# Kernel optimization log

Measured on AMD Instinct MI355X. Metric: run time of the kernel, lower is better.

## Reference

```python
import jax, jax.numpy as jnp
import numpy as np

B, L, H, D = 2, 2048, 16, 64
HID = H * D
EPS = 1e-6


def setup_inputs() -> dict:
    key = jax.random.key(0)
    k1, k2, k3 = jax.random.split(key, 3)
    x = jax.random.normal(k1, (B, L, HID), dtype=jnp.float32)
    Wqkv = jax.random.normal(k2, (HID, 3 * HID), dtype=jnp.float32) * 0.02
    Wo = jax.random.normal(k3, (HID, HID), dtype=jnp.float32) * 0.02
    q_norm_w = jnp.ones((D,), dtype=jnp.float32)
    k_norm_w = jnp.ones((D,), dtype=jnp.float32)
    # real RoPE tables: (L, D/2)
    d2 = D // 2
    inv_freq = 1.0 / (10000.0 ** (np.arange(d2, dtype=np.float32) / d2))
    ang = np.arange(L, dtype=np.float32)[:, None] * inv_freq[None, :]
    cos = jnp.asarray(np.cos(ang), dtype=jnp.float32)
    sin = jnp.asarray(np.sin(ang), dtype=jnp.float32)
    return {"x": x, "Wqkv": Wqkv, "Wo": Wo, "q_norm_w": q_norm_w,
            "k_norm_w": k_norm_w, "cos": cos, "sin": sin}


def _rmsnorm(t, w, eps=EPS):
    # normalize over last (head_dim) axis
    var = jnp.mean(t * t, axis=-1, keepdims=True)
    return t * jax.lax.rsqrt(var + eps) * w


def _rope(t, cos, sin):
    # t: (B,H,L,D); cos,sin: (1,1,L,D/2)
    d2 = t.shape[-1] // 2
    t1, t2 = t[..., :d2], t[..., d2:]
    return jnp.concatenate([t1 * cos - t2 * sin, t1 * sin + t2 * cos], axis=-1)


def reference(x, Wqkv, Wo, q_norm_w, k_norm_w, cos, sin):
    Bx, Lx, _ = x.shape
    qkv = x @ Wqkv                                   # (B,L,3*HID)
    qkv = qkv.reshape(Bx, Lx, 3, H, D)
    q = jnp.transpose(qkv[:, :, 0], (0, 2, 1, 3))    # (B,H,L,D)
    k = jnp.transpose(qkv[:, :, 1], (0, 2, 1, 3))
    v = jnp.transpose(qkv[:, :, 2], (0, 2, 1, 3))
    q = _rmsnorm(q, q_norm_w)
    k = _rmsnorm(k, k_norm_w)
    c = cos[:Lx][None, None]                         # (1,1,L,D/2)
    s = sin[:Lx][None, None]
    q = _rope(q, c, s)
    k = _rope(k, c, s)
    scale = 1.0 / jnp.sqrt(jnp.float32(D))
    scores = jnp.einsum("bhqd,bhkd->bhqk", q, k) * scale
    causal = jnp.tril(jnp.ones((Lx, Lx), dtype=bool))
    scores = jnp.where(causal, scores, jnp.finfo(scores.dtype).min)
    attn = jax.nn.softmax(scores, axis=-1)
    out = jnp.einsum("bhqk,bhkd->bhqd", attn, v)     # (B,H,L,D)
    out = jnp.transpose(out, (0, 2, 1, 3)).reshape(Bx, Lx, HID)
    return out @ Wo
```

## Files before the change

### kernel.cpp

```cpp
#include <hip/hip_runtime.h>
#include <hip/hip_bf16.h>

typedef __attribute__((ext_vector_type(8))) short bh8;
typedef __attribute__((ext_vector_type(4))) float f4;

typedef unsigned short u16;
typedef unsigned int u32;

__device__ inline u16 f2b(float f) {
  __hip_bfloat16 h = __float2bfloat16(f);
  union { __hip_bfloat16 h; u16 u; } v; v.h = h; return v.u;
}
__device__ inline float b2f(u16 b) {
  union { u32 u; float f; } v; v.u = ((u32)b) << 16;
  return v.f;
}

__device__ __forceinline__ void gload16(const u16* g, u16* l) {
  __builtin_amdgcn_global_load_lds(
      (__attribute__((address_space(1))) void*)(g),
      (__attribute__((address_space(3))) void*)(l),
      16, 0, 0);
}

__global__ __launch_bounds__(256) void k_prep1(const float* __restrict__ x,
                                               const float* __restrict__ Wqkv,
                                               const float* __restrict__ Wo,
                                               u16* __restrict__ xb,
                                               u16* __restrict__ wqkvT,
                                               u16* __restrict__ woT) {
  int idx = blockIdx.x;
  if (idx < 4096) {
    int i = (idx * 256 + threadIdx.x) * 4;
    float4 v = *(const float4*)&x[i];
    ushort4 o;
    o.x = f2b(v.x); o.y = f2b(v.y); o.z = f2b(v.z); o.w = f2b(v.w);
    *(ushort4*)&xb[i] = o;
    return;
  }
  __shared__ u16 t[32][33];
  const float* W; u16* WT; int K, N, bxi, byi;
  if (idx < 7168) {
    int id2 = idx - 4096;
    W = Wqkv; WT = wqkvT; K = 1024; N = 3072;
    bxi = id2 % 96; byi = id2 / 96;
  } else {
    int id2 = idx - 7168;
    W = Wo; WT = woT; K = 1024; N = 1024;
    bxi = id2 & 31; byi = id2 >> 5;
  }
  int bx = bxi * 32, by = byi * 32;
  int xx = threadIdx.x & 31, yy = threadIdx.x >> 5;
  for (int j = 0; j < 4; ++j) {
    int r = yy + j * 8;
    t[r][xx] = f2b(W[(size_t)(by + r) * N + bx + xx]);
  }
  __syncthreads();
  for (int j = 0; j < 4; ++j) {
    int r = yy + j * 8;
    WT[(size_t)(bx + r) * K + by + xx] = t[xx][r];
  }
}

template <bool F32OUT>
__global__ __launch_bounds__(256) void k_gemm(const u16* __restrict__ A,
                                              const u16* __restrict__ Bt,
                                              void* __restrict__ Cout,
                                              int M, int N, int K) {
  __shared__ u16 As[2][128 * 64];
  __shared__ u16 Bs[2][128 * 64];
  const int tid = threadIdx.x;
  const int lane = tid & 63, wid = tid >> 6;
  const int l15 = lane & 15, lg = lane >> 4;

  int nwg = gridDim.x * gridDim.y;
  int bid = blockIdx.y * gridDim.x + blockIdx.x;
  int cpx = nwg >> 3;
  int swz = (bid & 7) * cpx + (bid >> 3);
  int bx = swz % gridDim.x, by = swz / gridDim.x;
  const int bm = bx * 128, bn = by * 128;
  const int wr = (wid >> 1) * 64, wc = (wid & 1) * 64;

  f4 acc[4][4] = {};

  const int srow = wid * 32 + (lane >> 3);
  const int scol = (lane & 7) * 8;
  const u16* gA = A  + (size_t)(bm + srow) * K + scol;
  const u16* gB = Bt + (size_t)(bn + srow) * K + scol;

  const int nk = K >> 6;

  {
    const u16* ga = gA; const u16* gb = gB;
    u16* la = &As[0][(wid * 32) * 64];
    u16* lb = &Bs[0][(wid * 32) * 64];
    #pragma unroll
    for (int c = 0; c < 4; ++c) {
      gload16(ga, la);
      gload16(gb, lb);
      ga += (size_t)8 * K; gb += (size_t)8 * K;
      la += 8 * 64;        lb += 8 * 64;
    }
  }
  __syncthreads();

  for (int t = 0; t < nk; ++t) {
    if (t + 1 < nk) {
      int kb = (t + 1) << 6;
      const u16* ga = gA + kb; const u16* gb = gB + kb;
      u16* la = &As[(t + 1) & 1][(wid * 32) * 64];
      u16* lb = &Bs[(t + 1) & 1][(wid * 32) * 64];
      #pragma unroll
      for (int c = 0; c < 4; ++c) {
        gload16(ga, la);
        gload16(gb, lb);
        ga += (size_t)8 * K; gb += (size_t)8 * K;
        la += 8 * 64;        lb += 8 * 64;
      }
    }
    const u16* as = &As[t & 1][0];
    const u16* bs = &Bs[t & 1][0];
    #pragma unroll
    for (int kk = 0; kk < 2; ++kk) {
      bh8 a[4], b[4];
      #pragma unroll
      for (int m = 0; m < 4; ++m)
        a[m] = *(const bh8*)&as[(wr + m * 16 + l15) * 64 + kk * 32 + lg * 8];
      #pragma unroll
      for (int n = 0; n < 4; ++n)
        b[n] = *(const bh8*)&bs[(wc + n * 16 + l15) * 64 + kk * 32 + lg * 8];
      #pragma unroll
      for (int m = 0; m < 4; ++m)
        #pragma unroll
        for (int n = 0; n < 4; ++n)
          acc[m][n] = __builtin_amdgcn_mfma_f32_16x16x32_bf16(a[m], b[n], acc[m][n], 0, 0, 0);
    }
    __syncthreads();
  }

  for (int m = 0; m < 4; ++m)
    for (int n = 0; n < 4; ++n)
      for (int r = 0; r < 4; ++r) {
        int row = bm + wr + m * 16 + lg * 4 + r;
        int col = bn + wc + n * 16 + l15;
        float v = acc[m][n][r];
        if constexpr (F32OUT) ((float*)Cout)[(size_t)row * N + col] = v;
        else                  ((u16*)Cout)[(size_t)row * N + col]  = f2b(v);
      }
}

__global__ __launch_bounds__(256) void k_prep2(const u16* __restrict__ qkv,
                                               const float* __restrict__ qw,
                                               const float* __restrict__ kw,
                                               const float* __restrict__ cosp,
                                               const float* __restrict__ sinp,
                                               u16* __restrict__ Q,
                                               u16* __restrict__ K,
                                               u16* __restrict__ Vt) {
  const float CSC = 0.125f * 1.44269504088896f;
  int idx = blockIdx.x;
  if (idx < 2048) {
    int wid = threadIdx.x >> 6, lane = threadIdx.x & 63;
    int gw = idx * 4 + wid;
    int isK = gw & 1;
    int bl = gw >> 1;
    int l = bl & 2047, b = bl >> 11;
    int h = lane >> 2, qd = lane & 3;
    const u16* src = qkv + (size_t)bl * 3072 + isK * 1024 + h * 64 + qd * 8;
    bh8 t1 = *(const bh8*)src;
    bh8 t2 = *(const bh8*)(src + 32);
    float a1[8], a2[8];
    float ss = 0.0f;
    #pragma unroll
    for (int j = 0; j < 8; ++j) {
      a1[j] = b2f((u16)t1[j]); a2[j] = b2f((u16)t2[j]);
      ss += a1[j] * a1[j] + a2[j] * a2[j];
    }
    ss += __shfl_xor(ss, 1, 64);
    ss += __shfl_xor(ss, 2, 64);
    float rr = rsqrtf(ss * (1.0f / 64.0f) + 1e-6f);
    const float* wt = isK ? kw : qw;
    float w1[8], w2[8], cc[8], sn[8];
    *(float4*)&w1[0] = *(const float4*)&wt[qd * 8];
    *(float4*)&w1[4] = *(const float4*)&wt[qd * 8 + 4];
    *(float4*)&w2[0] = *(const float4*)&wt[32 + qd * 8];
    *(float4*)&w2[4] = *(const float4*)&wt[32 + qd * 8 + 4];
    *(float4*)&cc[0] = *(const float4*)&cosp[l * 32 + qd * 8];
    *(float4*)&cc[4] = *(const float4*)&cosp[l * 32 + qd * 8 + 4];
    *(float4*)&sn[0] = *(const float4*)&sinp[l * 32 + qd * 8];
    *(float4*)&sn[4] = *(const float4*)&sinp[l * 32 + qd * 8 + 4];
    float scl = isK ? 1.0f : CSC;
    bh8 o1, o2;
    #pragma unroll
    for (int j = 0; j < 8; ++j) {
      float x1 = a1[j] * rr * w1[j];
      float x2 = a2[j] * rr * w2[j];
      o1[j] = (short)f2b((x1 * cc[j] - x2 * sn[j]) * scl);
      o2[j] = (short)f2b((x1 * sn[j] + x2 * cc[j]) * scl);
    }
    u16* dst = (isK ? K : Q) + ((size_t)(b * 16 + h) * 2048 + l) * 64 + qd * 8;
    *(bh8*)dst = o1;
    *(bh8*)(dst + 32) = o2;
  } else {
    __shared__ u16 t[32][33];
    int v = idx - 2048;
    int bxi = v & 63, byi = (v >> 6) & 1, bh = v >> 7;
    int b = bh >> 4, h = bh & 15;
    int lb = bxi * 32, db = byi * 32;
    int xx = threadIdx.x & 31, yy = threadIdx.x >> 5;
    const u16* src = qkv + (size_t)b * 2048 * 3072 + 2048 + h * 64;
    for (int j = 0; j < 4; ++j) {
      int r = yy + j * 8;
      t[r][xx] = src[(size_t)(lb + r) * 3072 + db + xx];
    }
    __syncthreads();
    u16* dst = Vt + (size_t)bh * 64 * 2048;
    for (int j = 0; j < 4; ++j) {
      int r = yy + j * 8;
      dst[(size_t)(db + r) * 2048 + lb + xx] = t[xx][r];
    }
  }
}

__global__ __launch_bounds__(256, 3) void k_attn(const u16* __restrict__ Q,
                                                 const u16* __restrict__ K,
                                                 const u16* __restrict__ Vt,
                                                 u16* __restrict__ O,
                                                 u16* __restrict__ Opart,
                                                 float2* __restrict__ Ml) {
  __shared__ u16 Ks[2][64 * 64];
  __shared__ u16 Vs[2][64 * 64];
  __shared__ u16 Pl[4][32][64];

  const int bh = blockIdx.y;
  const int b = bh >> 4, h = bh & 15;
  const int wid = threadIdx.x >> 6, lane = threadIdx.x & 63;
  const int l15 = lane & 15, lg = lane >> 4;

  const int id = 39 - (int)blockIdx.x;
  int qt, t0, t1, slot;
  if (id < 4) { qt = id; t0 = 0; t1 = 2 * qt + 2; slot = -1; }
  else if (id < 12) {
    int p = id - 4; qt = 4 + (p >> 1); int half = p & 1;
    int nt = qt + 1; t0 = half * nt; t1 = t0 + nt;
    slot = bh * 36 + (qt - 4) * 2 + half;
  } else if (id < 24) {
    int p = id - 12; qt = 8 + p / 3; int part = p % 3;
    int T = 2 * qt + 2; t0 = part * T / 3; t1 = (part + 1) * T / 3;
    slot = bh * 36 + 8 + (qt - 8) * 3 + part;
  } else {
    int p = id - 24; qt = 12 + (p >> 2); int part = p & 3;
    int T = 2 * qt + 2; t0 = part * T / 4; t1 = (part + 1) * T / 4;
    slot = bh * 36 + 20 + (qt - 12) * 4 + part;
  }
  const int qb = qt * 128 + wid * 32;

  const u16* Qp = Q  + (size_t)bh * 2048 * 64;
  const u16* Kp = K  + (size_t)bh * 2048 * 64;
  const u16* Vp = Vt + (size_t)bh * 64 * 2048;

  const int sr0 = wid * 8 + (lane >> 3);
  const int sc  = lane & 7;

  bh8 aq[2][2];
  #pragma unroll
  for (int qi = 0; qi < 2; ++qi)
    #pragma unroll
    for (int hh = 0; hh < 2; ++hh)
      aq[qi][hh] = *(const bh8*)&Qp[(size_t)(qb + qi * 16 + l15) * 64 + hh * 32 + lg * 8];

  bh8 ones;
  #pragma unroll
  for (int j = 0; j < 8; ++j) ones[j] = (short)0x3F80;

  f4 acc[2][4] = {};
  float mrow[2] = {-1e30f, -1e30f};
  float lrow[2] = {0.0f, 0.0f};

  const int tmax = (qb + 31) >> 6;

  {
    int kb0 = t0 * 64;
    int r0 = sr0, r1 = 32 + sr0;
    gload16(Kp + (size_t)(kb0 + r0) * 64 + (size_t)((sc ^ (r0 & 7)) * 8), &Ks[t0 & 1][(wid * 8) * 64]);
    gload16(Kp + (size_t)(kb0 + r1) * 64 + (size_t)((sc ^ (r1 & 7)) * 8), &Ks[t0 & 1][(32 + wid * 8) * 64]);
    gload16(Vp + (size_t)r0 * 2048 + kb0 + (size_t)((sc ^ (r0 & 7)) * 8), &Vs[t0 & 1][(wid * 8) * 64]);
    gload16(Vp + (size_t)r1 * 2048 + kb0 + (size_t)((sc ^ (r1 & 7)) * 8), &Vs[t0 & 1][(32 + wid * 8) * 64]);
  }
  __syncthreads();

  for (int t = t0; t < t1; ++t) {
    if (t + 1 < t1) {
      int kb = (t + 1) * 64;
      int nb = (t + 1) & 1;
      int r0 = sr0, r1 = 32 + sr0;
      gload16(Kp + (size_t)(kb + r0) * 64 + (size_t)((sc ^ (r0 & 7)) * 8), &Ks[nb][(wid * 8) * 64]);
      gload16(Kp + (size_t)(kb + r1) * 64 + (size_t)((sc ^ (r1 & 7)) * 8), &Ks[nb][(32 + wid * 8) * 64]);
      gload16(Vp + (size_t)r0 * 2048 + kb + (size_t)((sc ^ (r0 & 7)) * 8), &Vs[nb][(wid * 8) * 64]);
      gload16(Vp + (size_t)r1 * 2048 + kb + (size_t)((sc ^ (r1 & 7)) * 8), &Vs[nb][(32 + wid * 8) * 64]);
    }
    if (t <= tmax) {
      const int kb = t * 64;
      const bool masked = (t == tmax);
      const u16* ks = &Ks[t & 1][0];
      const u16* vs = &Vs[t & 1][0];

      f4 sc4[4][2] = {};
      __builtin_amdgcn_s_setprio(1);
      #pragma unroll
      for (int kq = 0; kq < 4; ++kq) {
        int row = kq * 16 + l15;
        int cs = row & 7;
        bh8 ka0 = *(const bh8*)&ks[row * 64 + ((0 + lg) ^ cs) * 8];
        bh8 ka1 = *(const bh8*)&ks[row * 64 + ((4 + lg) ^ cs) * 8];
        #pragma unroll
        for (int qi = 0; qi < 2; ++qi) {
          sc4[kq][qi] = __builtin_amdgcn_mfma_f32_16x16x32_bf16(ka0, aq[qi][0], sc4[kq][qi], 0, 0, 0);
          sc4[kq][qi] = __builtin_amdgcn_mfma_f32_16x16x32_bf16(ka1, aq[qi][1], sc4[kq][qi], 0, 0, 0);
        }
      }
      __builtin_amdgcn_s_setprio(0);

      #pragma unroll
      for (int qi = 0; qi < 2; ++qi) {
        if (masked) {
          int q = qb + qi * 16 + l15;
          #pragma unroll
          for (int kq = 0; kq < 4; ++kq)
            #pragma unroll
            for (int r = 0; r < 4; ++r)
              if (kb + kq * 16 + lg * 4 + r > q) sc4[kq][qi][r] = -1e30f;
        }
        float mx = -1e30f;
        #pragma unroll
        for (int kq = 0; kq < 4; ++kq)
          #pragma unroll
          for (int r = 0; r < 4; ++r)
            mx = fmaxf(mx, sc4[kq][qi][r]);
        mx = fmaxf(mx, __shfl_xor(mx, 16, 64));
        mx = fmaxf(mx, __shfl_xor(mx, 32, 64));
        if (__any(mx > mrow[qi] + 8.0f)) {
          float mnew = fmaxf(mrow[qi], mx);
          float fac = exp2f(mrow[qi] - mnew);
          mrow[qi] = mnew;
          lrow[qi] *= fac;
          #pragma unroll
          for (int n = 0; n < 4; ++n)
            #pragma unroll
            for (int r = 0; r < 4; ++r) acc[qi][n][r] *= fac;
        }
        #pragma unroll
        for (int kq = 0; kq < 4; ++kq)
          #pragma unroll
          for (int r = 0; r < 4; ++r)
            sc4[kq][qi][r] = exp2f(sc4[kq][qi][r] - mrow[qi]);
      }

      char* plb = (char*)&Pl[wid][0][0];
      #pragma unroll
      for (int qi = 0; qi < 2; ++qi) {
        int row = qi * 16 + l15;
        #pragma unroll
        for (int kq = 0; kq < 4; ++kq) {
          ushort4 w4;
          w4.x = f2b(sc4[kq][qi][0]); w4.y = f2b(sc4[kq][qi][1]);
          w4.z = f2b(sc4[kq][qi][2]); w4.w = f2b(sc4[kq][qi][3]);
          int ch = (kq * 2 + (lg >> 1)) ^ (row & 7);
          *(ushort4*)(plb + row * 128 + ch * 16 + (lg & 1) * 8) = w4;
        }
      }
      asm volatile("s_waitcnt lgkmcnt(0)" ::: "memory");
      __builtin_amdgcn_sched_barrier(0);

      f4 sum0 = {}, sum1 = {};
      __builtin_amdgcn_s_setprio(1);
      #pragma unroll
      for (int g = 0; g < 2; ++g) {
        bh8 pb0 = *(const bh8*)(plb + l15 * 128 + (((g * 4 + lg) ^ (l15 & 7)) * 16));
        bh8 pb1 = *(const bh8*)(plb + (16 + l15) * 128 + (((g * 4 + lg) ^ (l15 & 7)) * 16));
        #pragma unroll
        for (int n = 0; n < 4; ++n) {
          int row = n * 16 + l15;
          bh8 va = *(const bh8*)&vs[row * 64 + (((g * 4 + lg) ^ (row & 7)) * 8)];
          acc[0][n] = __builtin_amdgcn_mfma_f32_16x16x32_bf16(va, pb0, acc[0][n], 0, 0, 0);
          acc[1][n] = __builtin_amdgcn_mfma_f32_16x16x32_bf16(va, pb1, acc[1][n], 0, 0, 0);
        }
        sum0 = __builtin_amdgcn_mfma_f32_16x16x32_bf16(ones, pb0, sum0, 0, 0, 0);
        sum1 = __builtin_amdgcn_mfma_f32_16x16x32_bf16(ones, pb1, sum1, 0, 0, 0);
      }
      __builtin_amdgcn_s_setprio(0);
      lrow[0] += sum0[0];
      lrow[1] += sum1[0];
    }
    __syncthreads();
  }

  if (slot < 0) {
    #pragma unroll
    for (int qi = 0; qi < 2; ++qi) {
      float inv = 1.0f / lrow[qi];
      int q = qb + qi * 16 + l15;
      #pragma unroll
      for (int n = 0; n < 4; ++n) {
        ushort4 w4;
        w4.x = f2b(acc[qi][n][0] * inv);
        w4.y = f2b(acc[qi][n][1] * inv);
        w4.z = f2b(acc[qi][n][2] * inv);
        w4.w = f2b(acc[qi][n][3] * inv);
        *(ushort4*)&O[((size_t)b * 2048 + q) * 1024 + h * 64 + n * 16 + lg * 4] = w4;
      }
    }
  } else {
    u16* op = Opart + (size_t)slot * 8192;
    #pragma unroll
    for (int qi = 0; qi < 2; ++qi) {
      int rloc = wid * 32 + qi * 16 + l15;
      #pragma unroll
      for (int n = 0; n < 4; ++n) {
        ushort4 w4;
        w4.x = f2b(acc[qi][n][0]); w4.y = f2b(acc[qi][n][1]);
        w4.z = f2b(acc[qi][n][2]); w4.w = f2b(acc[qi][n][3]);
        *(ushort4*)&op[(size_t)rloc * 64 + n * 16 + lg * 4] = w4;
      }
      if (lg == 0) Ml[slot * 128 + rloc] = make_float2(mrow[qi], lrow[qi]);
    }
  }
}

__global__ __launch_bounds__(256) void k_comb(const u16* __restrict__ Opart,
                                              const float2* __restrict__ Ml,
                                              u16* __restrict__ O) {
  int qt = 4 + (int)blockIdx.x;
  int bh = blockIdx.y;
  int b = bh >> 4, h = bh & 15;
  int ways = qt < 8 ? 2 : (qt < 12 ? 3 : 4);
  int base = bh * 36 + (qt < 8 ? (qt - 4) * 2 : qt < 12 ? 8 + (qt - 8) * 3 : 20 + (qt - 12) * 4);
  int row = threadIdx.x >> 1;
  int db  = (threadIdx.x & 1) * 32;

  float2 ml[4]; float wgt[4];
  float M = -1e30f;
  #pragma unroll
  for (int w = 0; w < 4; ++w)
    if (w < ways) { ml[w] = Ml[(base + w) * 128 + row]; M = fmaxf(M, ml[w].x); }
  float l = 0.0f;
  #pragma unroll
  for (int w = 0; w < 4; ++w)
    if (w < ways) { wgt[w] = exp2f(ml[w].x - M); l += wgt[w] * ml[w].y; }
  float inv = 1.0f / l;

  u16* dst = O + ((size_t)b * 2048 + qt * 128 + row) * 1024 + h * 64 + db;
  #pragma unroll
  for (int j = 0; j < 32; j += 8) {
    float a[8] = {};
    #pragma unroll
    for (int w = 0; w < 4; ++w)
      if (w < ways) {
        bh8 v = *(const bh8*)&Opart[(size_t)(base + w) * 8192 + (size_t)row * 64 + db + j];
        #pragma unroll
        for (int e = 0; e < 8; ++e) a[e] += wgt[w] * b2f((u16)v[e]);
      }
    bh8 o;
    #pragma unroll
    for (int e = 0; e < 8; ++e) o[e] = (short)f2b(a[e] * inv);
    *(bh8*)&dst[j] = o;
  }
}

extern "C" void kernel_launch(void* const* d_in, const int* in_sizes, int n_in,
                              void* d_out, int out_size, void* d_ws, size_t ws_size,
                              hipStream_t stream) {
  (void)in_sizes; (void)n_in; (void)out_size; (void)ws_size;
  const float* x    = (const float*)d_in[0];
  const float* Wqkv = (const float*)d_in[1];
  const float* Wo   = (const float*)d_in[2];
  const float* qw   = (const float*)d_in[3];
  const float* kw   = (const float*)d_in[4];
  const float* cosp = (const float*)d_in[5];
  const float* sinp = (const float*)d_in[6];
  float* out = (float*)d_out;

  char* ws = (char*)d_ws;
  u16* xb    = (u16*)(ws);
  u16* wqkvT = (u16*)(ws + 8388608);
  u16* woT   = (u16*)(ws + 14680064);
  u16* qkv   = (u16*)(ws + 16777216);
  u16* Qb    = (u16*)(ws + 41943040);
  u16* Kb    = (u16*)(ws + 50331648);
  u16* Vtb   = (u16*)(ws + 58720256);
  u16* AO    = (u16*)(ws + 67108864);
  u16*    Opart = (u16*)(ws + 16777216);
  float2* Mlb   = (float2*)(ws + 35651584);

  k_prep1<<<8192, 256, 0, stream>>>(x, Wqkv, Wo, xb, wqkvT, woT);
  k_gemm<false><<<dim3(32, 24), 256, 0, stream>>>(xb, wqkvT, qkv, 4096, 3072, 1024);
  k_prep2<<<6144, 256, 0, stream>>>(qkv, qw, kw, cosp, sinp, Qb, Kb, Vtb);
  k_attn<<<dim3(40, 32), 256, 0, stream>>>(Qb, Kb, Vtb, AO, Opart, Mlb);
  k_comb<<<dim3(12, 32), 256, 0, stream>>>(Opart, Mlb, AO);
  k_gemm<true><<<dim3(32, 8), 256, 0, stream>>>(AO, woT, out, 4096, 1024, 1024);
}
```

Baseline: 155.6 us.

## Add 256x256-tile 8-wave GEMM with swizzled LDS for QKV projection

Adds a new GEMM kernel with 256x256 output tiles, 512 threads (8 waves) and XOR-swizzled LDS rows to avoid bank conflicts. It uses it for the QKV projection, cutting the grid to 192 workgroups. Larger tiles increase operand reuse per LDS load and reduce global traffic. The trade-off is fewer workgroups than the 256 CUs, so some CUs sit idle, plus heavier register pressure. The old kernel loses its block-index swizzle, which only affects the output projection launch.

New measurement: 144.1 us. 1.08x faster.

```diff
diff --git a/kernel.cpp b/kernel.cpp
--- a/kernel.cpp
+++ b/kernel.cpp
@@ -63,6 +63,107 @@
 }
 
 template <bool F32OUT>
+__global__ __launch_bounds__(512, 2) void k_gemm256(const u16* __restrict__ A,
+                                                    const u16* __restrict__ Bt,
+                                                    void* __restrict__ Cout,
+                                                    int M, int N, int K) {
+  __shared__ u16 As[2][2][128 * 64];
+  __shared__ u16 Bs[2][2][128 * 64];
+  const int tid = threadIdx.x;
+  const int lane = tid & 63, wid = tid >> 6;
+  const int l15 = lane & 15, lg = lane >> 4;
+  const int wm = wid >> 2, wn = wid & 3;
+
+  int nwg = gridDim.x * gridDim.y;
+  int bid = blockIdx.y * gridDim.x + blockIdx.x;
+  int cpx = nwg >> 3;
+  int swz = (bid & 7) * cpx + (bid >> 3);
+  int bx = swz % gridDim.x, by = swz / gridDim.x;
+  const int bm = bx * 256, bn = by * 256;
+
+  f4 acc[8][4] = {};
+
+  const int srow = wid * 16 + (lane >> 3);
+  const int key0 = (lane >> 3) & 7;
+  const int scol = ((lane & 7) ^ key0) * 8;
+
+  const int nk = K >> 6;
+
+#define STAGE256(T)                                                                   \
+  {                                                                                   \
+    int kb_ = (T) << 6; int bf_ = (T) & 1;                                            \
+    _Pragma("unroll")                                                                 \
+    for (int h = 0; h < 2; ++h) {                                                     \
+      const u16* ga = A + (size_t)(bm + h * 128 + srow) * K + kb_ + scol;             \
+      u16* la = &As[bf_][h][(wid * 16) * 64];                                         \
+      gload16(ga, la);                                                                \
+      gload16(ga + (size_t)8 * K, la + 8 * 64);                                       \
+      const u16* gb = Bt + (size_t)(bn + h * 128 + srow) * K + kb_ + scol;            \
+      u16* lb = &Bs[bf_][h][(wid * 16) * 64];                                         \
+      gload16(gb, lb);                                                                \
+      gload16(gb + (size_t)8 * K, lb + 8 * 64);                                       \
+    }                                                                                 \
+  }
+
+#define QUAD256(T, MH, NH)                                                            \
+  {                                                                                   \
+    const u16* as_ = &As[(T) & 1][wm][0];                                             \
+    const u16* bs_ = &Bs[(T) & 1][wn >> 1][0];                                        \
+    bh8 a_[4][2], b_[2][2];                                                           \
+    _Pragma("unroll")                                                                 \
+    for (int i = 0; i < 4; ++i) {                                                     \
+      int ar = ((MH) * 4 + i) * 16 + l15;                                             \
+      _Pragma("unroll")                                                               \
+      for (int kk = 0; kk < 2; ++kk)                                                  \
+        a_[i][kk] = *(const bh8*)&as_[ar * 64 + (((kk * 4 + lg) ^ (ar & 7)) * 8)];    \
+    }                                                                                 \
+    _Pragma("unroll")                                                                 \
+    for (int j = 0; j < 2; ++j) {                                                     \
+      int br = (wn & 1) * 64 + ((NH) * 2 + j) * 16 + l15;                             \
+      _Pragma("unroll")                                                               \
+      for (int kk = 0; kk < 2; ++kk)                                                  \
+        b_[j][kk] = *(const bh8*)&bs_[br * 64 + (((kk * 4 + lg) ^ (br & 7)) * 8)];    \
+    }                                                                                 \
+    asm volatile("s_waitcnt lgkmcnt(0)" ::: "memory");                                \
+    __builtin_amdgcn_sched_barrier(0);                                                \
+    __builtin_amdgcn_s_setprio(1);                                                    \
+    _Pragma("unroll")                                                                 \
+    for (int kk = 0; kk < 2; ++kk)                                                    \
+      _Pragma("unroll")                                                               \
+      for (int i = 0; i < 4; ++i)                                                     \
+        _Pragma("unroll")                                                             \
+        for (int j = 0; j < 2; ++j)                                                   \
+          acc[(MH) * 4 + i][(NH) * 2 + j] = __builtin_amdgcn_mfma_f32_16x16x32_bf16(  \
+              a_[i][kk], b_[j][kk], acc[(MH) * 4 + i][(NH) * 2 + j], 0, 0, 0);        \
+    __builtin_amdgcn_s_setprio(0);                                                    \
+  }
+
+  STAGE256(0);
+  __syncthreads();
+
+  for (int t = 0; t < nk; ++t) {
+    if (t + 1 < nk) STAGE256(t + 1);
+    QUAD256(t, 0, 0);
+    QUAD256(t, 0, 1);
+    QUAD256(t, 1, 0);
+    QUAD256(t, 1, 1);
+    __syncthreads();
+  }
+#undef STAGE256
+#undef QUAD256
+
+  for (int mf = 0; mf < 8; ++mf)
+    for (int nf = 0; nf < 4; ++nf)
+      for (int r = 0; r < 4; ++r) {
+        int row = bm + wm * 128 + mf * 16 + lg * 4 + r;
+        int col = bn + wn * 64 + nf * 16 + l15;
+        float v = acc[mf][nf][r];
+        if constexpr (F32OUT) ((float*)Cout)[(size_t)row * N + col] = v;
+        else                  ((u16*)Cout)[(size_t)row * N + col]  = f2b(v);
+      }
+}
+
+template <bool F32OUT>
 __global__ __launch_bounds__(256) void k_gemm(const u16* __restrict__ A,
                                               const u16* __restrict__ Bt,
                                               void* __restrict__ Cout,
@@ -72,13 +173,7 @@
   const int tid = threadIdx.x;
   const int lane = tid & 63, wid = tid >> 6;
   const int l15 = lane & 15, lg = lane >> 4;
-
-  int nwg = gridDim.x * gridDim.y;
-  int bid = blockIdx.y * gridDim.x + blockIdx.x;
-  int cpx = nwg >> 3;
-  int swz = (bid & 7) * cpx + (bid >> 3);
-  int bx = swz % gridDim.x, by = swz / gridDim.x;
-  const int bm = bx * 128, bn = by * 128;
+  const int bm = blockIdx.x * 128, bn = blockIdx.y * 128;
   const int wr = (wid >> 1) * 64, wc = (wid & 1) * 64;
 
   f4 acc[4][4] = {};
@@ -493,7 +588,7 @@
   float2* Mlb   = (float2*)(ws + 35651584);
 
   k_prep1<<<8192, 256, 0, stream>>>(x, Wqkv, Wo, xb, wqkvT, woT);
-  k_gemm<false><<<dim3(32, 24), 256, 0, stream>>>(xb, wqkvT, qkv, 4096, 3072, 1024);
+  k_gemm256<false><<<dim3(16, 12), 512, 0, stream>>>(xb, wqkvT, qkv, 4096, 3072, 1024);
   k_prep2<<<6144, 256, 0, stream>>>(qkv, qw, kw, cosp, sinp, Qb, Kb, Vtb);
   k_attn<<<dim3(40, 32), 256, 0, stream>>>(Qb, Kb, Vtb, AO, Opart, Mlb);
   k_comb<<<dim3(12, 32), 256, 0, stream>>>(Opart, Mlb, AO);
```
